# Kernel optimization log

Measured on AMD Instinct MI355X. Metric: run time of the kernel, lower is better.

Reference implementation:

```python
import jax, jax.numpy as jnp
import numpy as np

NUM_HEADS = 12

def setup_inputs() -> dict:
    key = jax.random.key(0)
    ks = jax.random.split(key, 9)
    B, N, C = 4, 1024, 768
    hd = C // NUM_HEADS  # 64
    return {
        "x": jax.random.normal(ks[0], (B, N, C), dtype=jnp.float32),
        "prev_attn": jax.random.uniform(ks[1], (B, NUM_HEADS, N, N), dtype=jnp.float32) / N,
        "qkv_w": jax.random.normal(ks[2], (3 * C, C), dtype=jnp.float32) * 0.02,
        "proj_w": jax.random.normal(ks[3], (C, C), dtype=jnp.float32) * 0.02,
        "proj_b": jax.random.normal(ks[4], (C,), dtype=jnp.float32) * 0.02,
        "bp_w1": jax.random.normal(ks[5], (hd // 2, 2 * hd), dtype=jnp.float32) * 0.02,
        "bp_b1": jax.random.normal(ks[6], (hd // 2,), dtype=jnp.float32) * 0.02,
        "bp_w2": jax.random.normal(ks[7], (3, hd // 2), dtype=jnp.float32) * 0.02,
        "bp_b2": jax.random.normal(ks[8], (3,), dtype=jnp.float32) * 0.02,
    }

def reference(x, prev_attn, qkv_w, proj_w, proj_b, bp_w1, bp_b1, bp_w2, bp_b2):
    B, N, C = x.shape
    H = NUM_HEADS
    hd = C // H
    scale = hd ** -0.5
    # qkv projection: [B,N,3C] -> [3,B,H,N,hd]
    qkv = (x @ qkv_w.T).reshape(B, N, 3, H, hd).transpose(2, 0, 3, 1, 4)
    q, k, v = qkv[0], qkv[1], qkv[2]
    # scaled dot-product scores [B,H,N,N]
    attn_logits = jnp.einsum('bhnd,bhmd->bhnm', q, k) * scale
    cur_attn = jax.nn.softmax(attn_logits, axis=-1)
    # per-(b,h,n) bias MLP on concat(q,k): [B,H,N,2*hd] -> [B,H,N,3]
    qk = jnp.concatenate((q, k), axis=-1)
    h1 = jax.nn.relu(jnp.einsum('bhnd,od->bhno', qk, bp_w1) + bp_b1)
    bias = jnp.abs(jnp.einsum('bhno,po->bhnp', h1, bp_w2) + bp_b2)  # [B,H,N,3]
    # blend current attention, previous attention, and uniform term
    attn = (cur_attn * (1.0 + bias[..., 0:1])
            + prev_attn * bias[..., 1:2]
            - bias[..., 2:3] / N)
    out = jnp.einsum('bhnm,bhmd->bhnd', attn, v)  # [B,H,N,hd]
    out = out.transpose(0, 2, 1, 3).reshape(B, N, C)
    out = out @ proj_w.T + proj_b
    return (out, cur_attn)
```

## Files before the change

kernel.cpp:

```cpp
#include <hip/hip_runtime.h>

typedef __bf16 bf16_t;
typedef __bf16 bf16x8 __attribute__((ext_vector_type(8)));
typedef __bf16 bf16x4 __attribute__((ext_vector_type(4)));
typedef float f32x4 __attribute__((ext_vector_type(4)));

static constexpr int Bb = 4, Hh = 12, Nn = 1024, Cc = 768, HD = 64;
static constexpr int OUT0 = Bb * Nn * Cc;

#define GLD16(gp, lp)                                                       \
  __builtin_amdgcn_global_load_lds(                                         \
      (const __attribute__((address_space(1))) unsigned int*)(gp),          \
      (__attribute__((address_space(3))) unsigned int*)(lp), 16, 0, 0)

__global__ __launch_bounds__(256) void convert_all(
    const float* __restrict__ x, const float* __restrict__ qw, const float* __restrict__ pw,
    bf16_t* __restrict__ xb, bf16_t* __restrict__ qwb, bf16_t* __restrict__ pwb) {
  const int NX = (Bb * Nn * Cc) / 4;
  const int NQ = (3 * Cc * Cc) / 4;
  int i = blockIdx.x * 256 + threadIdx.x;
  const float4* src;
  bf16_t* dst;
  int off;
  if (i < NX) { src = (const float4*)x; dst = xb; off = i; }
  else if (i < NX + NQ) { src = (const float4*)qw; dst = qwb; off = i - NX; }
  else { src = (const float4*)pw; dst = pwb; off = i - NX - NQ; }
  float4 v = src[off];
  bf16x4 o;
  o[0] = (bf16_t)v.x; o[1] = (bf16_t)v.y; o[2] = (bf16_t)v.z; o[3] = (bf16_t)v.w;
  *(bf16x4*)(dst + (size_t)off * 4) = o;
}

__global__ __launch_bounds__(256) void gemm_qkv(
    const bf16_t* __restrict__ A, const bf16_t* __restrict__ Bm,
    bf16_t* __restrict__ q_bf, bf16_t* __restrict__ k_bf, bf16_t* __restrict__ vT_bf) {
  __shared__ bf16_t As[128 * 32];
  __shared__ bf16_t Bs[128 * 32];
  const int tid = threadIdx.x;
  const int lane = tid & 63;
  const int w = tid >> 6;
  const int wr = w >> 1, wc = w & 1;
  const int g = lane >> 4, r = lane & 15;
  const int m0 = (blockIdx.x / 18) << 7;
  const int n0 = (blockIdx.x % 18) << 7;

  const f32x4 fz = {0.f, 0.f, 0.f, 0.f};
  f32x4 acc[4][4];
#pragma unroll
  for (int i = 0; i < 4; i++)
#pragma unroll
    for (int j = 0; j < 4; j++) acc[i][j] = fz;

  for (int k0 = 0; k0 < 768; k0 += 32) {
#pragma unroll
    for (int c = 0; c < 2; c++) {
      int row = w * 32 + c * 16 + (lane >> 2);
      int kof = (lane & 3) << 3;
      GLD16(&A[(size_t)(m0 + row) * 768 + k0 + kof], (char*)As + w * 2048 + c * 1024);
      GLD16(&Bm[(size_t)(n0 + row) * 768 + k0 + kof], (char*)Bs + w * 2048 + c * 1024);
    }
    __syncthreads();
    bf16x8 af[4], bfv[4];
#pragma unroll
    for (int i = 0; i < 4; i++) af[i] = *(const bf16x8*)&As[(wr * 64 + i * 16 + r) * 32 + g * 8];
#pragma unroll
    for (int j = 0; j < 4; j++) bfv[j] = *(const bf16x8*)&Bs[(wc * 64 + j * 16 + r) * 32 + g * 8];
#pragma unroll
    for (int i = 0; i < 4; i++)
#pragma unroll
      for (int j = 0; j < 4; j++)
        acc[i][j] = __builtin_amdgcn_mfma_f32_16x16x32_bf16(af[i], bfv[j], acc[i][j], 0, 0, 0);
    __syncthreads();
  }

#pragma unroll
  for (int i = 0; i < 4; i++) {
#pragma unroll
    for (int j = 0; j < 4; j++) {
      int c = n0 + wc * 64 + j * 16 + r;
#pragma unroll
      for (int e = 0; e < 4; e++) {
        int mrow = m0 + wr * 64 + i * 16 + g * 4 + e;
        float val = acc[i][j][e];
        int which = c / 768;
        int cc = c - which * 768;
        int h = cc >> 6, d = cc & 63;
        int b = mrow >> 10, n = mrow & 1023;
        size_t bh = (size_t)(b * Hh + h);
        if (which == 0)      q_bf[(bh * Nn + n) * HD + d] = (bf16_t)val;
        else if (which == 1) k_bf[(bh * Nn + n) * HD + d] = (bf16_t)val;
        else                 vT_bf[(bh * HD + d) * Nn + n] = (bf16_t)val;
      }
    }
  }
}

template <int MODE>
__global__ __launch_bounds__(256) void gemm_bt(
    const bf16_t* __restrict__ A, const bf16_t* __restrict__ Bm, int N, int K,
    float* __restrict__ outF, const float* __restrict__ bias) {
  __shared__ bf16_t As[128 * 40];
  __shared__ bf16_t Bs[128 * 40];
  const int tid = threadIdx.x;
  const int lane = tid & 63;
  const int w = tid >> 6;
  const int wr = w >> 1, wc = w & 1;
  const int g = lane >> 4, r = lane & 15;
  const int ntiles = N >> 7;
  const int m0 = (blockIdx.x / ntiles) << 7;
  const int n0 = (blockIdx.x % ntiles) << 7;

  const f32x4 fz = {0.f, 0.f, 0.f, 0.f};
  f32x4 acc[4][4];
#pragma unroll
  for (int i = 0; i < 4; i++)
#pragma unroll
    for (int j = 0; j < 4; j++) acc[i][j] = fz;

  for (int k0 = 0; k0 < K; k0 += 32) {
#pragma unroll
    for (int p = 0; p < 2; p++) {
      int idx = tid + (p << 8);
      int row = idx >> 2;
      int kof = (idx & 3) << 3;
      *(bf16x8*)&As[row * 40 + kof] = *(const bf16x8*)&A[(size_t)(m0 + row) * K + k0 + kof];
      *(bf16x8*)&Bs[row * 40 + kof] = *(const bf16x8*)&Bm[(size_t)(n0 + row) * K + k0 + kof];
    }
    __syncthreads();
    bf16x8 af[4], bfv[4];
#pragma unroll
    for (int i = 0; i < 4; i++) af[i] = *(const bf16x8*)&As[(wr * 64 + i * 16 + r) * 40 + g * 8];
#pragma unroll
    for (int j = 0; j < 4; j++) bfv[j] = *(const bf16x8*)&Bs[(wc * 64 + j * 16 + r) * 40 + g * 8];
#pragma unroll
    for (int i = 0; i < 4; i++)
#pragma unroll
      for (int j = 0; j < 4; j++)
        acc[i][j] = __builtin_amdgcn_mfma_f32_16x16x32_bf16(af[i], bfv[j], acc[i][j], 0, 0, 0);
    __syncthreads();
  }

#pragma unroll
  for (int i = 0; i < 4; i++) {
#pragma unroll
    for (int j = 0; j < 4; j++) {
      int c = n0 + wc * 64 + j * 16 + r;
#pragma unroll
      for (int e = 0; e < 4; e++) {
        int mrow = m0 + wr * 64 + i * 16 + g * 4 + e;
        outF[(size_t)mrow * N + c] = acc[i][j][e] + bias[c];
      }
    }
  }
}

__global__ __launch_bounds__(256) void bias_mlp(
    const bf16_t* __restrict__ qb, const bf16_t* __restrict__ kb,
    const float* __restrict__ w1, const float* __restrict__ b1,
    const float* __restrict__ w2, const float* __restrict__ b2,
    float* __restrict__ bias4) {
  __shared__ float w1s[32 * 130];
  __shared__ float qks[8][128];
  __shared__ float h1s[8][32];
  const int t = threadIdx.x;
#pragma unroll
  for (int p = 0; p < 16; p++) {
    int idx = p * 256 + t;
    w1s[(idx >> 7) * 130 + (idx & 127)] = w1[idx];
  }
  const int rl = t >> 5, u = t & 31;
  const int rowg = blockIdx.x * 8 + rl;
  {
    int i4 = u * 4;
    const bf16_t* src = (i4 < 64) ? (qb + (size_t)rowg * HD + i4)
                                  : (kb + (size_t)rowg * HD + (i4 - 64));
    bf16x4 vv = *(const bf16x4*)src;
#pragma unroll
    for (int z = 0; z < 4; z++) qks[rl][i4 + z] = (float)vv[z];
  }
  __syncthreads();
  float accv = b1[u];
#pragma unroll 16
  for (int i2 = 0; i2 < 64; i2++) {
    float2 wv = *(const float2*)&w1s[u * 130 + i2 * 2];
    float2 qv = *(const float2*)&qks[rl][i2 * 2];
    accv += wv.x * qv.x + wv.y * qv.y;
  }
  h1s[rl][u] = fmaxf(accv, 0.f);
  __syncthreads();
  if (u < 4) {
    float outv = 0.f;
    if (u < 3) {
      float s = b2[u];
#pragma unroll
      for (int j = 0; j < 32; j++) s += w2[u * 32 + j] * h1s[rl][j];
      float v = fabsf(s);
      outv = (u == 0) ? (1.f + v) : ((u == 1) ? v : -v * (1.f / (float)Nn));
    }
    bias4[(size_t)rowg * 4 + u] = outv;
  }
}

__global__ __launch_bounds__(256, 3) void attn_fused(
    const bf16_t* __restrict__ qb, const bf16_t* __restrict__ kb,
    const bf16_t* __restrict__ vT, const float* __restrict__ prev,
    const float* __restrict__ bias4, float* __restrict__ cur,
    bf16_t* __restrict__ oh) {
  __shared__ char Plb[16 * 2048];
  __shared__ float redmax[16][4];
  __shared__ float redsum[16][4];
  const int bid = blockIdx.x;
  const int tile = (bid & 7) * 384 + (bid >> 3);
  const int bh = tile >> 6, mt = tile & 63;
  const int tid = threadIdx.x;
  const int lane = tid & 63, w = tid >> 6;
  const int g = lane >> 4, r = lane & 15;
  const int row0 = mt << 4;
  const int cbase = w << 8;

  const bf16_t* qp = qb + ((size_t)bh * Nn + row0) * HD;
  const bf16_t* kp = kb + (size_t)bh * Nn * HD;
  bf16x8 qr0 = *(const bf16x8*)&qp[r * HD + g * 8];
  bf16x8 qr1 = *(const bf16x8*)&qp[r * HD + g * 8 + 32];
  bf16x8 qa0, qa1;
#pragma unroll
  for (int j = 0; j < 8; j++) {
    qa0[j] = (bf16_t)((float)qr0[j] * 0.125f);
    qa1[j] = (bf16_t)((float)qr1[j] * 0.125f);
  }
  const f32x4 fz = {0.f, 0.f, 0.f, 0.f};
  f32x4 acc[16];
#pragma unroll
  for (int t = 0; t < 16; t++) {
    int col = cbase + (t << 4) + r;
    bf16x8 kf0 = *(const bf16x8*)&kp[(size_t)col * HD + g * 8];
    bf16x8 kf1 = *(const bf16x8*)&kp[(size_t)col * HD + g * 8 + 32];
    f32x4 z = __builtin_amdgcn_mfma_f32_16x16x32_bf16(kf0, qa0, fz, 0, 0, 0);
    acc[t] = __builtin_amdgcn_mfma_f32_16x16x32_bf16(kf1, qa1, z, 0, 0, 0);
  }

  const float* ppr = prev + (size_t)bh * Nn * Nn + (size_t)(row0 + r) * Nn + cbase + (g << 2);
  float4 pv[16];
#pragma unroll
  for (int t = 0; t < 16; t++) pv[t] = *(const float4*)&ppr[t << 4];

  float mj = -3.0e38f;
#pragma unroll
  for (int t = 0; t < 16; t++)
#pragma unroll
    for (int e = 0; e < 4; e++) mj = fmaxf(mj, acc[t][e]);
  mj = fmaxf(mj, __shfl_xor(mj, 16, 64));
  mj = fmaxf(mj, __shfl_xor(mj, 32, 64));
  if (lane < 16) redmax[lane][w] = mj;
  __syncthreads();
  float rm;
  {
    float v0 = fmaxf(redmax[r][0], redmax[r][1]);
    rm = fmaxf(v0, fmaxf(redmax[r][2], redmax[r][3]));
  }
  float sj = 0.f;
#pragma unroll
  for (int t = 0; t < 16; t++)
#pragma unroll
    for (int e = 0; e < 4; e++) {
      float ev = __expf(acc[t][e] - rm);
      acc[t][e] = ev;
      sj += ev;
    }
  sj += __shfl_xor(sj, 16, 64);
  sj += __shfl_xor(sj, 32, 64);
  if (lane < 16) redsum[lane][w] = sj;
  __syncthreads();
  const float inv =
      1.f / (redsum[r][0] + redsum[r][1] + redsum[r][2] + redsum[r][3]);

  const float4 bvr = *(const float4*)&bias4[((size_t)bh * 1024 + row0 + r) * 4];
  const float b0c = bvr.x, b1c = bvr.y, b2c = bvr.z;
  float* cp = cur + (size_t)bh * Nn * Nn + (size_t)(row0 + r) * Nn + cbase + (g << 2);
#pragma unroll
  for (int t = 0; t < 16; t++) {
    float4 p;
    p.x = acc[t][0] * inv;
    p.y = acc[t][1] * inv;
    p.z = acc[t][2] * inv;
    p.w = acc[t][3] * inv;
    *(float4*)&cp[t << 4] = p;
    bf16x4 nb;
    nb[0] = (bf16_t)(b0c * p.x + b1c * pv[t].x + b2c);
    nb[1] = (bf16_t)(b0c * p.y + b1c * pv[t].y + b2c);
    nb[2] = (bf16_t)(b0c * p.z + b1c * pv[t].z + b2c);
    nb[3] = (bf16_t)(b0c * p.w + b1c * pv[t].w + b2c);
    int col = cbase + (t << 4) + (g << 2);
    int off = (r * 2048 + col * 2) ^ ((r & 7) << 4);
    *(bf16x4*)(Plb + off) = nb;
  }
  __syncthreads();

  const bf16_t* vrow = vT + (size_t)bh * HD * Nn + (size_t)((w << 4) + r) * Nn;
  f32x4 c0 = fz, c1 = fz, c2 = fz, c3 = fz;
#pragma unroll
  for (int ks = 0; ks < 8; ks++) {
    int kA = ks << 5;
    bf16x8 pA = *(const bf16x8*)(Plb + ((r * 2048 + (kA + g * 8) * 2) ^ ((r & 7) << 4)));
    bf16x8 pB = *(const bf16x8*)(Plb + ((r * 2048 + (256 + kA + g * 8) * 2) ^ ((r & 7) << 4)));
    bf16x8 pC = *(const bf16x8*)(Plb + ((r * 2048 + (512 + kA + g * 8) * 2) ^ ((r & 7) << 4)));
    bf16x8 pD = *(const bf16x8*)(Plb + ((r * 2048 + (768 + kA + g * 8) * 2) ^ ((r & 7) << 4)));
    bf16x8 vA = *(const bf16x8*)&vrow[kA + g * 8];
    bf16x8 vB = *(const bf16x8*)&vrow[256 + kA + g * 8];
    bf16x8 vC = *(const bf16x8*)&vrow[512 + kA + g * 8];
    bf16x8 vD = *(const bf16x8*)&vrow[768 + kA + g * 8];
    c0 = __builtin_amdgcn_mfma_f32_16x16x32_bf16(pA, vA, c0, 0, 0, 0);
    c1 = __builtin_amdgcn_mfma_f32_16x16x32_bf16(pB, vB, c1, 0, 0, 0);
    c2 = __builtin_amdgcn_mfma_f32_16x16x32_bf16(pC, vC, c2, 0, 0, 0);
    c3 = __builtin_amdgcn_mfma_f32_16x16x32_bf16(pD, vD, c3, 0, 0, 0);
  }
  f32x4 osum = (c0 + c1) + (c2 + c3);
  const int b = bh / Hh, h = bh % Hh;
#pragma unroll
  for (int e = 0; e < 4; e++) {
    int nrow = row0 + g * 4 + e;
    oh[((size_t)(b * Nn + nrow)) * Cc + h * HD + (w << 4) + r] = (bf16_t)osum[e];
  }
}

extern "C" void kernel_launch(void* const* d_in, const int* in_sizes, int n_in,
                              void* d_out, int out_size, void* d_ws, size_t ws_size,
                              hipStream_t stream) {
  const float* x      = (const float*)d_in[0];
  const float* prev   = (const float*)d_in[1];
  const float* qkv_w  = (const float*)d_in[2];
  const float* proj_w = (const float*)d_in[3];
  const float* proj_b = (const float*)d_in[4];
  const float* bp_w1  = (const float*)d_in[5];
  const float* bp_b1  = (const float*)d_in[6];
  const float* bp_w2  = (const float*)d_in[7];
  const float* bp_w2b = (const float*)d_in[8];

  float* out0 = (float*)d_out;
  float* cur  = out0 + OUT0;

  char* ws = (char*)d_ws;
  bf16_t* xb    = (bf16_t*)(ws + 0);
  bf16_t* qwb   = (bf16_t*)(ws + 6291456);
  bf16_t* pwb   = (bf16_t*)(ws + 9830400);
  bf16_t* qbf   = (bf16_t*)(ws + 11010048);
  bf16_t* kbf   = (bf16_t*)(ws + 17301504);
  bf16_t* vtb   = (bf16_t*)(ws + 23592960);
  float*  bias4 = (float*)(ws + 29884416);
  bf16_t* ohb   = (bf16_t*)(ws + 30670848);
  if (ws_size < 36962304) return;

  convert_all<<<5376, 256, 0, stream>>>(x, qkv_w, proj_w, xb, qwb, pwb);
  gemm_qkv<<<32 * 18, 256, 0, stream>>>(xb, qwb, qbf, kbf, vtb);
  bias_mlp<<<49152 / 8, 256, 0, stream>>>(qbf, kbf, bp_w1, bp_b1, bp_w2, bp_w2b, bias4);
  attn_fused<<<3072, 256, 0, stream>>>(qbf, kbf, vtb, prev, bias4, cur, ohb);
  gemm_bt<1><<<(4096 / 128) * (768 / 128), 256, 0, stream>>>(
      ohb, pwb, 768, 768, out0, proj_b);
}
```

Measured before the change: 247.3 us.

## Process 32 query rows per attention block to reuse K and V loads

The fused attention kernel now handles two 16-row query tiles per block, so each K fragment and each V fragment loaded from global memory feeds twice as many MFMAs. The grid is halved, shared memory for the probability tile doubles, and launch bounds drop to two blocks per CU. The unnormalised exponentials are now kept in registers as bf16 and the prev_attn loads are deferred into the write loop, which lowers register pressure but rounds the written cur_attn values through bf16 before normalisation. The costs are lower occupancy and less latency hiding on the memory-bound prev and cur streams.

```diff
diff --git a/kernel.cpp b/kernel.cpp
--- a/kernel.cpp
+++ b/kernel.cpp
@@ -201,125 +201,186 @@
   }
 }
 
-__global__ __launch_bounds__(256, 3) void attn_fused(
+__global__ __launch_bounds__(256, 2) void attn_fused(
     const bf16_t* __restrict__ qb, const bf16_t* __restrict__ kb,
     const bf16_t* __restrict__ vT, const float* __restrict__ prev,
     const float* __restrict__ bias4, float* __restrict__ cur,
     bf16_t* __restrict__ oh) {
-  __shared__ char Plb[16 * 2048];
-  __shared__ float redmax[16][4];
-  __shared__ float redsum[16][4];
+  __shared__ char Plb[32 * 2048];
+  __shared__ float redmax[32][4];
+  __shared__ float redsum[32][4];
   const int bid = blockIdx.x;
-  const int tile = (bid & 7) * 384 + (bid >> 3);
-  const int bh = tile >> 6, mt = tile & 63;
+  const int tile = (bid & 7) * 192 + (bid >> 3);
+  const int bh = tile >> 5, mt = tile & 31;
   const int tid = threadIdx.x;
   const int lane = tid & 63, w = tid >> 6;
   const int g = lane >> 4, r = lane & 15;
-  const int row0 = mt << 4;
+  const int row0 = mt << 5;
   const int cbase = w << 8;
 
   const bf16_t* qp = qb + ((size_t)bh * Nn + row0) * HD;
   const bf16_t* kp = kb + (size_t)bh * Nn * HD;
-  bf16x8 qr0 = *(const bf16x8*)&qp[r * HD + g * 8];
-  bf16x8 qr1 = *(const bf16x8*)&qp[r * HD + g * 8 + 32];
-  bf16x8 qa0, qa1;
+  bf16x8 q00 = *(const bf16x8*)&qp[r * HD + g * 8];
+  bf16x8 q01 = *(const bf16x8*)&qp[r * HD + g * 8 + 32];
+  bf16x8 q10 = *(const bf16x8*)&qp[(16 + r) * HD + g * 8];
+  bf16x8 q11 = *(const bf16x8*)&qp[(16 + r) * HD + g * 8 + 32];
+  bf16x8 qa0, qa1, qb0, qb1;
 #pragma unroll
   for (int j = 0; j < 8; j++) {
-    qa0[j] = (bf16_t)((float)qr0[j] * 0.125f);
-    qa1[j] = (bf16_t)((float)qr1[j] * 0.125f);
+    qa0[j] = (bf16_t)((float)q00[j] * 0.125f);
+    qa1[j] = (bf16_t)((float)q01[j] * 0.125f);
+    qb0[j] = (bf16_t)((float)q10[j] * 0.125f);
+    qb1[j] = (bf16_t)((float)q11[j] * 0.125f);
   }
   const f32x4 fz = {0.f, 0.f, 0.f, 0.f};
-  f32x4 acc[16];
+  f32x4 acc0[16], acc1[16];
 #pragma unroll
   for (int t = 0; t < 16; t++) {
     int col = cbase + (t << 4) + r;
     bf16x8 kf0 = *(const bf16x8*)&kp[(size_t)col * HD + g * 8];
     bf16x8 kf1 = *(const bf16x8*)&kp[(size_t)col * HD + g * 8 + 32];
-    f32x4 z = __builtin_amdgcn_mfma_f32_16x16x32_bf16(kf0, qa0, fz, 0, 0, 0);
-    acc[t] = __builtin_amdgcn_mfma_f32_16x16x32_bf16(kf1, qa1, z, 0, 0, 0);
-  }
-
-  const float* ppr = prev + (size_t)bh * Nn * Nn + (size_t)(row0 + r) * Nn + cbase + (g << 2);
-  float4 pv[16];
-#pragma unroll
-  for (int t = 0; t < 16; t++) pv[t] = *(const float4*)&ppr[t << 4];
-
-  float mj = -3.0e38f;
+    f32x4 z0 = __builtin_amdgcn_mfma_f32_16x16x32_bf16(kf0, qa0, fz, 0, 0, 0);
+    acc0[t] = __builtin_amdgcn_mfma_f32_16x16x32_bf16(kf1, qa1, z0, 0, 0, 0);
+    f32x4 z1 = __builtin_amdgcn_mfma_f32_16x16x32_bf16(kf0, qb0, fz, 0, 0, 0);
+    acc1[t] = __builtin_amdgcn_mfma_f32_16x16x32_bf16(kf1, qb1, z1, 0, 0, 0);
+  }
+
+  float mj0 = -3.0e38f, mj1 = -3.0e38f;
 #pragma unroll
   for (int t = 0; t < 16; t++)
 #pragma unroll
-    for (int e = 0; e < 4; e++) mj = fmaxf(mj, acc[t][e]);
-  mj = fmaxf(mj, __shfl_xor(mj, 16, 64));
-  mj = fmaxf(mj, __shfl_xor(mj, 32, 64));
-  if (lane < 16) redmax[lane][w] = mj;
+    for (int e = 0; e < 4; e++) {
+      mj0 = fmaxf(mj0, acc0[t][e]);
+      mj1 = fmaxf(mj1, acc1[t][e]);
+    }
+  mj0 = fmaxf(mj0, __shfl_xor(mj0, 16, 64));
+  mj0 = fmaxf(mj0, __shfl_xor(mj0, 32, 64));
+  mj1 = fmaxf(mj1, __shfl_xor(mj1, 16, 64));
+  mj1 = fmaxf(mj1, __shfl_xor(mj1, 32, 64));
+  if (lane < 16) {
+    redmax[lane][w] = mj0;
+    redmax[16 + lane][w] = mj1;
+  }
   __syncthreads();
-  float rm;
+  float rm0, rm1;
   {
     float v0 = fmaxf(redmax[r][0], redmax[r][1]);
-    rm = fmaxf(v0, fmaxf(redmax[r][2], redmax[r][3]));
-  }
-  float sj = 0.f;
-#pragma unroll
-  for (int t = 0; t < 16; t++)
-#pragma unroll
-    for (int e = 0; e < 4; e++) {
-      float ev = __expf(acc[t][e] - rm);
-      acc[t][e] = ev;
-      sj += ev;
-    }
-  sj += __shfl_xor(sj, 16, 64);
-  sj += __shfl_xor(sj, 32, 64);
-  if (lane < 16) redsum[lane][w] = sj;
+    rm0 = fmaxf(v0, fmaxf(redmax[r][2], redmax[r][3]));
+    float v1 = fmaxf(redmax[16 + r][0], redmax[16 + r][1]);
+    rm1 = fmaxf(v1, fmaxf(redmax[16 + r][2], redmax[16 + r][3]));
+  }
+  float sj0 = 0.f, sj1 = 0.f;
+  bf16x4 p0[16], p1[16];
+#pragma unroll
+  for (int t = 0; t < 16; t++) {
+    float a0 = __expf(acc0[t][0] - rm0), a1 = __expf(acc0[t][1] - rm0);
+    float a2 = __expf(acc0[t][2] - rm0), a3 = __expf(acc0[t][3] - rm0);
+    sj0 += (a0 + a1) + (a2 + a3);
+    p0[t][0] = (bf16_t)a0; p0[t][1] = (bf16_t)a1;
+    p0[t][2] = (bf16_t)a2; p0[t][3] = (bf16_t)a3;
+    float b0v = __expf(acc1[t][0] - rm1), b1v = __expf(acc1[t][1] - rm1);
+    float b2v = __expf(acc1[t][2] - rm1), b3v = __expf(acc1[t][3] - rm1);
+    sj1 += (b0v + b1v) + (b2v + b3v);
+    p1[t][0] = (bf16_t)b0v; p1[t][1] = (bf16_t)b1v;
+    p1[t][2] = (bf16_t)b2v; p1[t][3] = (bf16_t)b3v;
+  }
+  sj0 += __shfl_xor(sj0, 16, 64);
+  sj0 += __shfl_xor(sj0, 32, 64);
+  sj1 += __shfl_xor(sj1, 16, 64);
+  sj1 += __shfl_xor(sj1, 32, 64);
+  if (lane < 16) {
+    redsum[lane][w] = sj0;
+    redsum[16 + lane][w] = sj1;
+  }
   __syncthreads();
-  const float inv =
+  const float inv0 =
       1.f / (redsum[r][0] + redsum[r][1] + redsum[r][2] + redsum[r][3]);
-
-  const float4 bvr = *(const float4*)&bias4[((size_t)bh * 1024 + row0 + r) * 4];
-  const float b0c = bvr.x, b1c = bvr.y, b2c = bvr.z;
-  float* cp = cur + (size_t)bh * Nn * Nn + (size_t)(row0 + r) * Nn + cbase + (g << 2);
-#pragma unroll
-  for (int t = 0; t < 16; t++) {
-    float4 p;
-    p.x = acc[t][0] * inv;
-    p.y = acc[t][1] * inv;
-    p.z = acc[t][2] * inv;
-    p.w = acc[t][3] * inv;
-    *(float4*)&cp[t << 4] = p;
-    bf16x4 nb;
-    nb[0] = (bf16_t)(b0c * p.x + b1c * pv[t].x + b2c);
-    nb[1] = (bf16_t)(b0c * p.y + b1c * pv[t].y + b2c);
-    nb[2] = (bf16_t)(b0c * p.z + b1c * pv[t].z + b2c);
-    nb[3] = (bf16_t)(b0c * p.w + b1c * pv[t].w + b2c);
-    int col = cbase + (t << 4) + (g << 2);
-    int off = (r * 2048 + col * 2) ^ ((r & 7) << 4);
-    *(bf16x4*)(Plb + off) = nb;
+  const float inv1 =
+      1.f / (redsum[16 + r][0] + redsum[16 + r][1] + redsum[16 + r][2] + redsum[16 + r][3]);
+
+  const float4 bv0 = *(const float4*)&bias4[((size_t)bh * 1024 + row0 + r) * 4];
+  const float4 bv1 = *(const float4*)&bias4[((size_t)bh * 1024 + row0 + 16 + r) * 4];
+  {
+    const float* ppr = prev + (size_t)bh * Nn * Nn + (size_t)(row0 + r) * Nn + cbase + (g << 2);
+    float* cp = cur + (size_t)bh * Nn * Nn + (size_t)(row0 + r) * Nn + cbase + (g << 2);
+#pragma unroll
+    for (int t = 0; t < 16; t++) {
+      float4 pvv = *(const float4*)&ppr[t << 4];
+      float4 p;
+      p.x = (float)p0[t][0] * inv0;
+      p.y = (float)p0[t][1] * inv0;
+      p.z = (float)p0[t][2] * inv0;
+      p.w = (float)p0[t][3] * inv0;
+      *(float4*)&cp[t << 4] = p;
+      bf16x4 nb;
+      nb[0] = (bf16_t)(bv0.x * p.x + bv0.y * pvv.x + bv0.z);
+      nb[1] = (bf16_t)(bv0.x * p.y + bv0.y * pvv.y + bv0.z);
+      nb[2] = (bf16_t)(bv0.x * p.z + bv0.y * pvv.z + bv0.z);
+      nb[3] = (bf16_t)(bv0.x * p.w + bv0.y * pvv.w + bv0.z);
+      int col = cbase + (t << 4) + (g << 2);
+      int off = (r * 2048 + col * 2) ^ ((r & 7) << 4);
+      *(bf16x4*)(Plb + off) = nb;
+    }
+  }
+  {
+    const float* ppr = prev + (size_t)bh * Nn * Nn + (size_t)(row0 + 16 + r) * Nn + cbase + (g << 2);
+    float* cp = cur + (size_t)bh * Nn * Nn + (size_t)(row0 + 16 + r) * Nn + cbase + (g << 2);
+#pragma unroll
+    for (int t = 0; t < 16; t++) {
+      float4 pvv = *(const float4*)&ppr[t << 4];
+      float4 p;
+      p.x = (float)p1[t][0] * inv1;
+      p.y = (float)p1[t][1] * inv1;
+      p.z = (float)p1[t][2] * inv1;
+      p.w = (float)p1[t][3] * inv1;
+      *(float4*)&cp[t << 4] = p;
+      bf16x4 nb;
+      nb[0] = (bf16_t)(bv1.x * p.x + bv1.y * pvv.x + bv1.z);
+      nb[1] = (bf16_t)(bv1.x * p.y + bv1.y * pvv.y + bv1.z);
+      nb[2] = (bf16_t)(bv1.x * p.z + bv1.y * pvv.z + bv1.z);
+      nb[3] = (bf16_t)(bv1.x * p.w + bv1.y * pvv.w + bv1.z);
+      int col = cbase + (t << 4) + (g << 2);
+      int off = ((16 + r) * 2048 + col * 2) ^ ((r & 7) << 4);
+      *(bf16x4*)(Plb + off) = nb;
+    }
   }
   __syncthreads();
 
   const bf16_t* vrow = vT + (size_t)bh * HD * Nn + (size_t)((w << 4) + r) * Nn;
-  f32x4 c0 = fz, c1 = fz, c2 = fz, c3 = fz;
+  f32x4 o0q0 = fz, o0q1 = fz, o0q2 = fz, o0q3 = fz;
+  f32x4 o1q0 = fz, o1q1 = fz, o1q2 = fz, o1q3 = fz;
 #pragma unroll
   for (int ks = 0; ks < 8; ks++) {
     int kA = ks << 5;
-    bf16x8 pA = *(const bf16x8*)(Plb + ((r * 2048 + (kA + g * 8) * 2) ^ ((r & 7) << 4)));
-    bf16x8 pB = *(const bf16x8*)(Plb + ((r * 2048 + (256 + kA + g * 8) * 2) ^ ((r & 7) << 4)));
-    bf16x8 pC = *(const bf16x8*)(Plb + ((r * 2048 + (512 + kA + g * 8) * 2) ^ ((r & 7) << 4)));
-    bf16x8 pD = *(const bf16x8*)(Plb + ((r * 2048 + (768 + kA + g * 8) * 2) ^ ((r & 7) << 4)));
-    bf16x8 vA = *(const bf16x8*)&vrow[kA + g * 8];
-    bf16x8 vB = *(const bf16x8*)&vrow[256 + kA + g * 8];
-    bf16x8 vC = *(const bf16x8*)&vrow[512 + kA + g * 8];
-    bf16x8 vD = *(const bf16x8*)&vrow[768 + kA + g * 8];
-    c0 = __builtin_amdgcn_mfma_f32_16x16x32_bf16(pA, vA, c0, 0, 0, 0);
-    c1 = __builtin_amdgcn_mfma_f32_16x16x32_bf16(pB, vB, c1, 0, 0, 0);
-    c2 = __builtin_amdgcn_mfma_f32_16x16x32_bf16(pC, vC, c2, 0, 0, 0);
-    c3 = __builtin_amdgcn_mfma_f32_16x16x32_bf16(pD, vD, c3, 0, 0, 0);
-  }
-  f32x4 osum = (c0 + c1) + (c2 + c3);
+#pragma unroll
+    for (int q = 0; q < 4; q++) {
+      int k0 = (q << 8) + kA;
+      bf16x8 vb = *(const bf16x8*)&vrow[k0 + g * 8];
+      bf16x8 pa0 = *(const bf16x8*)(Plb + ((r * 2048 + (k0 + g * 8) * 2) ^ ((r & 7) << 4)));
+      bf16x8 pa1 = *(const bf16x8*)(Plb + (((16 + r) * 2048 + (k0 + g * 8) * 2) ^ ((r & 7) << 4)));
+      if (q == 0) {
+        o0q0 = __builtin_amdgcn_mfma_f32_16x16x32_bf16(pa0, vb, o0q0, 0, 0, 0);
+        o1q0 = __builtin_amdgcn_mfma_f32_16x16x32_bf16(pa1, vb, o1q0, 0, 0, 0);
+      } else if (q == 1) {
+        o0q1 = __builtin_amdgcn_mfma_f32_16x16x32_bf16(pa0, vb, o0q1, 0, 0, 0);
+        o1q1 = __builtin_amdgcn_mfma_f32_16x16x32_bf16(pa1, vb, o1q1, 0, 0, 0);
+      } else if (q == 2) {
+        o0q2 = __builtin_amdgcn_mfma_f32_16x16x32_bf16(pa0, vb, o0q2, 0, 0, 0);
+        o1q2 = __builtin_amdgcn_mfma_f32_16x16x32_bf16(pa1, vb, o1q2, 0, 0, 0);
+      } else {
+        o0q3 = __builtin_amdgcn_mfma_f32_16x16x32_bf16(pa0, vb, o0q3, 0, 0, 0);
+        o1q3 = __builtin_amdgcn_mfma_f32_16x16x32_bf16(pa1, vb, o1q3, 0, 0, 0);
+      }
+    }
+  }
+  f32x4 os0 = (o0q0 + o0q1) + (o0q2 + o0q3);
+  f32x4 os1 = (o1q0 + o1q1) + (o1q2 + o1q3);
   const int b = bh / Hh, h = bh % Hh;
 #pragma unroll
   for (int e = 0; e < 4; e++) {
     int nrow = row0 + g * 4 + e;
-    oh[((size_t)(b * Nn + nrow)) * Cc + h * HD + (w << 4) + r] = (bf16_t)osum[e];
+    oh[((size_t)(b * Nn + nrow)) * Cc + h * HD + (w << 4) + r] = (bf16_t)os0[e];
+    oh[((size_t)(b * Nn + nrow + 16)) * Cc + h * HD + (w << 4) + r] = (bf16_t)os1[e];
   }
 }
 
@@ -353,7 +414,7 @@
   convert_all<<<5376, 256, 0, stream>>>(x, qkv_w, proj_w, xb, qwb, pwb);
   gemm_qkv<<<32 * 18, 256, 0, stream>>>(xb, qwb, qbf, kbf, vtb);
   bias_mlp<<<49152 / 8, 256, 0, stream>>>(qbf, kbf, bp_w1, bp_b1, bp_w2, bp_w2b, bias4);
-  attn_fused<<<3072, 256, 0, stream>>>(qbf, kbf, vtb, prev, bias4, cur, ohb);
+  attn_fused<<<1536, 256, 0, stream>>>(qbf, kbf, vtb, prev, bias4, cur, ohb);
   gemm_bt<1><<<(4096 / 128) * (768 / 128), 256, 0, stream>>>(
       ohb, pwb, 768, 768, out0, proj_b);
 }
```

Result: faster. 226.0 us (-8.6%).
